# Optimization experiments

Measured on AMD Instinct MI355X. Metric: run time of the kernel, lower is better.

The kernel has to match this reference:

```python
import jax, jax.numpy as jnp
import numpy as np

DIM_V = 512
NUM_HEADS = 8
LN_EPS = 1e-5


def _layernorm(x):
    # LayerNorm over last dim, no affine (simplified_layer_norm=True)
    mu = jnp.mean(x, axis=-1, keepdims=True)
    var = jnp.mean(jnp.square(x - mu), axis=-1, keepdims=True)
    return (x - mu) * jax.lax.rsqrt(var + LN_EPS)


def setup_inputs() -> dict:
    key = jax.random.key(0)
    ks = jax.random.split(key, 12)
    B, Nq, Nk, dQ, dK, dV = 16, 1024, 1024, 512, 512, DIM_V
    s = 0.02
    return {
        "Q": jax.random.normal(ks[0], (B, Nq, dQ), jnp.float32),
        "K": jax.random.normal(ks[1], (B, Nk, dK), jnp.float32),
        "Wq": jax.random.normal(ks[2], (dQ, dV), jnp.float32) * s,
        "bq": jnp.zeros((dV,), jnp.float32),
        "Wk": jax.random.normal(ks[3], (dK, dV), jnp.float32) * s,
        "bk": jnp.zeros((dV,), jnp.float32),
        "Wv": jax.random.normal(ks[4], (dK, dV), jnp.float32) * s,
        "bv": jnp.zeros((dV,), jnp.float32),
        "Wo": jax.random.normal(ks[5], (dV, dV), jnp.float32) * s,
        "bo": jnp.zeros((dV,), jnp.float32),
    }


def reference(Q, K, Wq, bq, Wk, bk, Wv, bv, Wo, bo):
    H = NUM_HEADS
    dh = DIM_V // H
    q = Q @ Wq + bq            # [B, Nq, dV]
    k = K @ Wk + bk            # [B, Nk, dV]
    v = K @ Wv + bv            # [B, Nk, dV]
    B, Nq, _ = q.shape
    Nk = k.shape[1]
    qh = q.reshape(B, Nq, H, dh)
    kh = k.reshape(B, Nk, H, dh)
    vh = v.reshape(B, Nk, H, dh)
    # NOTE: faithful to source — scale by sqrt(dim_V), not sqrt(head_dim)
    scores = jnp.einsum('bqhd,bkhd->bhqk', qh, kh) / jnp.sqrt(jnp.asarray(DIM_V, q.dtype))
    A = jax.nn.softmax(scores, axis=-1)                    # [B, H, Nq, Nk]
    attn = jnp.einsum('bhqk,bkhd->bqhd', A, vh).reshape(B, Nq, DIM_V)
    O = q + attn               # residual with projected Q
    O = _layernorm(O)          # ln0 (no affine)
    O = O + jax.nn.gelu(O @ Wo + bo, approximate=False)
    O = _layernorm(O)          # ln1 (no affine)
    return O
```

## Files before the change

kernel.cpp:

```cpp
#include <hip/hip_runtime.h>
#include <hip/hip_bf16.h>
#include <math.h>

typedef __bf16 bf16;
typedef __bf16 bf16x8 __attribute__((ext_vector_type(8)));
typedef float  f32x4  __attribute__((ext_vector_type(4)));
typedef float  f32x16 __attribute__((ext_vector_type(16)));
typedef unsigned u32x4 __attribute__((ext_vector_type(4)));

#define MFMA16(a,b,c) __builtin_amdgcn_mfma_f32_16x16x32_bf16((a),(b),(c),0,0,0)
#define MFMA32(a,b,c) __builtin_amdgcn_mfma_f32_32x32x16_bf16((a),(b),(c),0,0,0)
#define KSCALE 0.0637587159f

__device__ __forceinline__ void async16p(const void* g, void* l) {
    __builtin_amdgcn_global_load_lds((const __attribute__((address_space(1))) void*)g,
                                     (__attribute__((address_space(3))) void*)l,
                                     16, 0, 0);
}

__device__ __forceinline__ float fexp2(float x) {
#if __has_builtin(__builtin_amdgcn_exp2f)
    return __builtin_amdgcn_exp2f(x);
#else
    return exp2f(x);
#endif
}

__device__ __forceinline__ unsigned pkbf(float a, float b) {
    union { bf16 h[2]; unsigned u; } x;
    x.h[0] = (bf16)a; x.h[1] = (bf16)b; return x.u;
}

__device__ __forceinline__ void plswap(unsigned &a, unsigned &b) {
#if __has_builtin(__builtin_amdgcn_permlane32_swap)
    auto r = __builtin_amdgcn_permlane32_swap((int)a, (int)b, false, false);
    a = (unsigned)r[0]; b = (unsigned)r[1];
#else
    unsigned sa = (unsigned)__shfl_xor((int)a, 32);
    unsigned sb = (unsigned)__shfl_xor((int)b, 32);
    bool hi = (threadIdx.x & 32) != 0;
    unsigned na = hi ? sb : a;
    unsigned nb = hi ? b  : sa;
    a = na; b = nb;
#endif
}

__global__ __launch_bounds__(256) void prep_w_kernel(
    const float* __restrict__ Wq, const float* __restrict__ Wk,
    const float* __restrict__ Wv, const float* __restrict__ Wo,
    bf16* __restrict__ WqT, bf16* __restrict__ WkT,
    bf16* __restrict__ WvT, bf16* __restrict__ WoT,
    float* __restrict__ csum)
{
    __shared__ float tile[32][33];
    const int bx = blockIdx.x;
    const float* W; bf16* T;
    switch (bx >> 8) {
      case 0: W=Wq; T=WqT; break;
      case 1: W=Wk; T=WkT; break;
      case 2: W=Wv; T=WvT; break;
      default: W=Wo; T=WoT; break;
    }
    const int rest = bx & 255;
    const int k0 = (rest & 15) * 32, n0 = (rest >> 4) * 32;
    const int tx = threadIdx.x & 31, ty = threadIdx.x >> 5;
    float sacc = 0.f;
    #pragma unroll
    for (int i=0;i<32;i+=8) {
        float v = W[(size_t)(k0+ty+i)*512 + n0+tx];
        tile[ty+i][tx] = v;
        sacc += v;
    }
    __syncthreads();
    #pragma unroll
    for (int i=0;i<32;i+=8)
        T[(size_t)(n0+ty+i)*512 + k0+tx] = (bf16)tile[tx][ty+i];
    if ((bx >> 8) == 3) {
        __syncthreads();
        tile[ty][tx] = sacc;
        __syncthreads();
        if (ty == 0) {
            float s = 0.f;
            #pragma unroll
            for (int j=0;j<8;j++) s += tile[j][tx];
            atomicAdd(&csum[n0+tx], s);
        }
    }
}

__global__ __launch_bounds__(256, 2) void gemm_proj_kernel(
    const float* __restrict__ Qf, const float* __restrict__ Kf,
    const bf16* __restrict__ WqT, const bf16* __restrict__ WkT,
    const bf16* __restrict__ WvT,
    const float* __restrict__ bq, const float* __restrict__ bk,
    const float* __restrict__ bv,
    bf16* __restrict__ qbb, bf16* __restrict__ kbb, bf16* __restrict__ vT)
{
    __shared__ __align__(16) char smem[65536];
    float* As32 = (float*)smem;
    bf16*  Bs   = (bf16*)(smem + 32768);
    bf16*  Lt   = (bf16*)smem;

    const int x = blockIdx.x;
    const bool isQ = (x < 256);
    int m0, n0;
    const float* A; const bf16 *BT0, *BT1; const float *bb0, *bb1;
    if (isQ) {
        m0 = (x >> 1) * 128; n0 = (x & 1) * 128;
        A = Qf; BT0 = WqT + (size_t)n0*512; BT1 = WqT + (size_t)(n0+256)*512;
        bb0 = bq + n0; bb1 = bq + n0 + 256;
    } else {
        int r = x - 256;
        m0 = (r >> 2) * 128; n0 = (r & 3) * 128;
        A = Kf; BT0 = WkT + (size_t)n0*512; BT1 = WvT + (size_t)n0*512;
        bb0 = bk + n0; bb1 = bv + n0;
    }

    const int tid = threadIdx.x;
    const int lane = tid & 63, wave = tid >> 6;
    const int qd = lane >> 4, lr = lane & 15;
    const int wm = (wave & 1) * 64, wn = (wave >> 1) * 64;

    const float* gA = A + (size_t)(m0 + (tid>>3))*512 + (((tid&7)^((tid>>3)&7))*4);
    const int bgr = ((tid & 3) ^ ((tid >> 3) & 3)) * 8;
    const bf16* gB0 = BT0 + (size_t)(tid>>2)*512 + bgr;
    const bf16* gB1 = BT1 + (size_t)(tid>>2)*512 + bgr;

    f32x4 acc[2][4][4];
    #pragma unroll
    for (int p=0;p<2;p++)
      #pragma unroll
      for (int i=0;i<4;i++)
        #pragma unroll
        for (int j=0;j<4;j++) acc[p][i][j] = (f32x4){0,0,0,0};

    auto stage = [&](int buf, int k0) {
        float* lA = As32 + buf*4096 + wave*256;
        #pragma unroll
        for (int i=0;i<4;i++)
            async16p(gA + k0 + (size_t)i*32*512, lA + i*1024);
        bf16* lB0 = Bs + buf*8192 + wave*512;
        async16p(gB0 + k0,                  lB0);
        async16p(gB0 + k0 + (size_t)64*512, lB0 + 2048);
        bf16* lB1 = Bs + buf*8192 + 4096 + wave*512;
        async16p(gB1 + k0,                  lB1);
        async16p(gB1 + k0 + (size_t)64*512, lB1 + 2048);
    };

    stage(0, 0);
    for (int t = 0; t < 16; ++t) {
        const int cur = t & 1;
        __builtin_amdgcn_sched_barrier(0);
        __builtin_amdgcn_s_barrier();
        if (t < 15) {
            stage(cur ^ 1, (t+1)*32);
            asm volatile("s_waitcnt vmcnt(8)" ::: "memory");
        } else {
            asm volatile("s_waitcnt vmcnt(0)" ::: "memory");
        }
        __builtin_amdgcn_s_barrier();

        const float* Ab = As32 + cur*4096;
        const bf16*  Bb = Bs   + cur*8192;
        bf16x8 af[4], bfr[2][4];
        #pragma unroll
        for (int mi=0;mi<4;mi++) {
            int row = wm + mi*16 + lr;
            f32x4 f0 = *(f32x4*)(Ab + row*32 + (((qd*2  )^(lr&7))*4));
            f32x4 f1 = *(f32x4*)(Ab + row*32 + (((qd*2+1)^(lr&7))*4));
            bf16x8 a;
            a[0]=(bf16)f0[0]; a[1]=(bf16)f0[1]; a[2]=(bf16)f0[2]; a[3]=(bf16)f0[3];
            a[4]=(bf16)f1[0]; a[5]=(bf16)f1[1]; a[6]=(bf16)f1[2]; a[7]=(bf16)f1[3];
            af[mi] = a;
        }
        #pragma unroll
        for (int p=0;p<2;p++)
          #pragma unroll
          for (int ni=0;ni<4;ni++)
            bfr[p][ni] = *(bf16x8*)(Bb + p*4096 + (wn+ni*16+lr)*32
                                       + ((qd^((lr>>1)&3))*8));
        #pragma unroll
        for (int p=0;p<2;p++)
          #pragma unroll
          for (int mi=0;mi<4;mi++)
            #pragma unroll
            for (int ni=0;ni<4;ni++)
              acc[p][mi][ni] = MFMA16(af[mi], bfr[p][ni], acc[p][mi][ni]);
    }

    if (isQ) {
        #pragma unroll
        for (int p=0;p<2;p++) {
            const float* bb = p ? bb1 : bb0;
            #pragma unroll
            for (int ni=0;ni<4;ni++) {
                int nl = wn + ni*16 + lr;
                int n = n0 + p*256 + nl;
                float bv0 = bb[nl];
                #pragma unroll
                for (int mi=0;mi<4;mi++) {
                    int mb = m0 + wm + mi*16 + qd*4;
                    #pragma unroll
                    for (int r=0;r<4;r++)
                        qbb[(size_t)(mb+r)*512 + n] = (bf16)(acc[p][mi][ni][r] + bv0);
                }
            }
        }
    } else {
        #pragma unroll
        for (int ni=0;ni<4;ni++) {
            int nl = wn + ni*16 + lr;
            int n = n0 + nl;
            float bv0 = bb0[nl];
            #pragma unroll
            for (int mi=0;mi<4;mi++) {
                int mb = m0 + wm + mi*16 + qd*4;
                #pragma unroll
                for (int r=0;r<4;r++)
                    kbb[(size_t)(mb+r)*512 + n] = (bf16)((acc[0][mi][ni][r] + bv0)*KSCALE);
            }
        }
        const int b = m0 >> 10, tok0 = m0 & 1023;
        const int row = tid >> 2, ch = tid & 3;
        #pragma unroll
        for (int half = 0; half < 2; ++half) {
            __syncthreads();
            if ((wn >> 6) == half) {
                #pragma unroll
                for (int ni=0;ni<4;ni++) {
                    int nl = ni*16 + lr;
                    float bvv = bb1[half*64 + nl];
                    #pragma unroll
                    for (int mi=0;mi<4;mi++)
                      #pragma unroll
                      for (int r=0;r<4;r++) {
                        int col = wm + mi*16 + qd*4 + r;
                        Lt[nl*128 + ((((col>>3)^(nl&7))<<3) | (col&7))]
                            = (bf16)(acc[1][mi][ni][r] + bvv);
                      }
                }
            }
            __syncthreads();
            const int h = (n0 >> 6) + half;
            bf16* dst = vT + ((size_t)((b*8 + h)*64 + row))*1024 + tok0 + ch*32;
            #pragma unroll
            for (int s=0;s<4;s++) {
                int g = (ch*4 + s) ^ (row & 7);
                *(uint4*)(dst + s*8) = *(uint4*)(Lt + row*128 + g*8);
            }
        }
    }
}

__global__ __launch_bounds__(256, 4) void attn_kernel(
    const bf16* __restrict__ qb, const bf16* __restrict__ kb,
    const bf16* __restrict__ vT, bf16* __restrict__ attnb)
{
    const int x = blockIdx.x;
    const int qt = x >> 7, h = x & 7, b = (x & 127) >> 3;
    const int tid = threadIdx.x, lane = tid & 63, wave = tid >> 6;
    const int l = lane & 31, hi = lane >> 5;
    const int q0w = qt*128 + wave*32;

    __shared__ __align__(16) bf16 kv[2][2][4096];
    __shared__ float ls[4][32];

    bf16x8 aq[4];
    {
        const bf16* qrow = qb + ((size_t)(b*1024 + q0w + l))*512 + h*64 + hi*8;
        #pragma unroll
        for (int st=0; st<4; ++st) aq[st] = *(const bf16x8*)(qrow + st*16);
    }

    const int srow = lane >> 3;
    const int sgA  = (lane & 7) ^ srow ^ wave;
    const int sgB  = sgA ^ 4;
    const bf16* kg0 = kb + ((size_t)(b*1024 + wave*8 + srow))*512      + h*64 + sgA*8;
    const bf16* kg1 = kb + ((size_t)(b*1024 + wave*8 + srow + 32))*512 + h*64 + sgB*8;
    const bf16* vg0 = vT + ((size_t)((b*8 + h)*64 + wave*8 + srow))*1024      + sgA*8;
    const bf16* vg1 = vT + ((size_t)((b*8 + h)*64 + wave*8 + srow + 32))*1024 + sgB*8;

    auto stage = [&](int buf, int t) {
        const size_t ko = (size_t)t*64*512;
        async16p(kg0 + ko,     &kv[buf][0][wave*512]);
        async16p(kg1 + ko,     &kv[buf][0][2048 + wave*512]);
        async16p(vg0 + t*64,   &kv[buf][1][wave*512]);
        async16p(vg1 + t*64,   &kv[buf][1][2048 + wave*512]);
    };

    f32x16 accO[2];
    accO[0] = (f32x16)0.f; accO[1] = (f32x16)0.f;
    float lsum = 0.f;
    const int kx = (l & 7) ^ (l >> 3);

    stage(0, 0);
    for (int t=0; t<16; ++t) {
        const int cur = t & 1;
        __builtin_amdgcn_sched_barrier(0);
        __builtin_amdgcn_s_barrier();
        if (t < 15) {
            stage(cur ^ 1, t + 1);
            asm volatile("s_waitcnt vmcnt(4)" ::: "memory");
        } else {
            asm volatile("s_waitcnt vmcnt(0)" ::: "memory");
        }
        __builtin_amdgcn_s_barrier();

        const bf16* Ks = kv[cur][0];
        const bf16* Vs = kv[cur][1];

        u32x4 paf[4];
        #pragma unroll
        for (int kb2=0; kb2<2; ++kb2) {
            f32x16 sT = (f32x16)0.f;
            __builtin_amdgcn_s_setprio(1);
            #pragma unroll
            for (int st=0; st<4; ++st) {
                bf16x8 kf = *(const bf16x8*)(Ks + (kb2*32 + l)*64
                               + (((st*2 + hi) ^ kx ^ (kb2<<2))*8));
                sT = MFMA32(kf, aq[st], sT);
            }
            __builtin_amdgcn_s_setprio(0);
            unsigned u[8];
            #pragma unroll
            for (int m=0; m<8; ++m) {
                float e0 = fexp2(sT[2*m]);
                float e1 = fexp2(sT[2*m+1]);
                lsum += e0 + e1;
                u[m] = pkbf(e0, e1);
            }
            #pragma unroll
            for (int sb=0; sb<2; ++sb) {
                unsigned a0=u[4*sb], a1=u[4*sb+1], a2=u[4*sb+2], a3=u[4*sb+3];
                plswap(a0, a2);
                plswap(a1, a3);
                paf[kb2*2 + sb] = (u32x4){a0, a1, a2, a3};
            }
        }
        __builtin_amdgcn_s_setprio(1);
        #pragma unroll
        for (int db=0; db<2; ++db) {
            f32x16 a = accO[db];
            #pragma unroll
            for (int st=0; st<4; ++st) {
                bf16x8 vf = *(const bf16x8*)(Vs + (db*32 + l)*64
                               + (((st*2 + hi) ^ kx ^ (db<<2))*8));
                u32x4 pp = paf[st];
                bf16x8 pf = *(bf16x8*)&pp;
                a = MFMA32(pf, vf, a);
            }
            accO[db] = a;
        }
        __builtin_amdgcn_s_setprio(0);
    }

    lsum += __shfl_xor(lsum, 32);
    ls[wave][l] = lsum;
    __syncthreads();

    #pragma unroll
    for (int g=0; g<4; ++g) {
        f32x4 lv = *(const f32x4*)(&ls[wave][g*8 + hi*4]);
        f32x4 inv;
        #pragma unroll
        for (int i=0;i<4;i++) inv[i] = 1.f / lv[i];
        #pragma unroll
        for (int db=0; db<2; ++db) {
            #pragma unroll
            for (int i=0;i<4;i++) {
                int r = g*4 + i;
                int qrow = q0w + g*8 + hi*4 + i;
                size_t idx = ((size_t)(b*1024 + qrow))*512 + h*64 + db*32 + l;
                float o = accO[db][r] * inv[i] + (float)qb[idx];
                attnb[idx] = (bf16)o;
            }
        }
    }
}

__global__ __launch_bounds__(256, 4) void gemm_o_kernel(
    const bf16* __restrict__ attnb, const bf16* __restrict__ WoT,
    const float* __restrict__ bo, const float* __restrict__ csum,
    bf16* __restrict__ xb)
{
    __shared__ __align__(16) char smem[24576];
    __shared__ float2 rs[64];
    bf16* As = (bf16*)smem;
    bf16* Bs = (bf16*)(smem + 8192);
    const int m0 = blockIdx.x * 64, n0 = blockIdx.y * 128;
    const int tid = threadIdx.x;
    const int lane = tid & 63, wave = tid >> 6;
    const int qd = lane >> 4, lr = lane & 15;
    const int wm = (wave & 1) * 32, wn = (wave >> 1) * 64;

    const int bgr = ((tid & 3) ^ ((tid >> 3) & 3)) * 8;
    const bf16* gA = attnb + (size_t)(m0 + (tid>>2))*512 + bgr;
    const bf16* gB = WoT   + (size_t)(n0 + (tid>>2))*512 + bgr;

    f32x4 acc[2][4];
    #pragma unroll
    for (int i=0;i<2;i++)
      #pragma unroll
      for (int j=0;j<4;j++) acc[i][j] = (f32x4){0,0,0,0};
    float s1[2] = {0.f, 0.f}, s2[2] = {0.f, 0.f};

    auto stage = [&](int buf, int k0) {
        async16p(gA + k0,                  As + buf*2048 + wave*512);
        bf16* lB = Bs + buf*4096 + wave*512;
        async16p(gB + k0,                  lB);
        async16p(gB + k0 + (size_t)64*512, lB + 2048);
    };

    stage(0, 0);
    for (int t = 0; t < 16; ++t) {
        const int cur = t & 1;
        __builtin_amdgcn_sched_barrier(0);
        __builtin_amdgcn_s_barrier();
        if (t < 15) {
            stage(cur ^ 1, (t+1)*32);
            asm volatile("s_waitcnt vmcnt(3)" ::: "memory");
        } else {
            asm volatile("s_waitcnt vmcnt(0)" ::: "memory");
        }
        __builtin_amdgcn_s_barrier();

        const bf16* Ab = As + cur*2048;
        const bf16* Bb = Bs + cur*4096;
        bf16x8 af[2], bfr[4];
        #pragma unroll
        for (int mi=0;mi<2;mi++) {
            af[mi] = *(bf16x8*)(Ab + (wm+mi*16+lr)*32 + ((qd^((lr>>1)&3))*8));
            #pragma unroll
            for (int j=0;j<8;j++) {
                float v = (float)af[mi][j];
                s1[mi] += v;
                s2[mi] += v*v;
            }
        }
        #pragma unroll
        for (int ni=0;ni<4;ni++)
            bfr[ni] = *(bf16x8*)(Bb + (wn+ni*16+lr)*32 + ((qd^((lr>>1)&3))*8));
        #pragma unroll
        for (int mi=0;mi<2;mi++)
          #pragma unroll
          for (int ni=0;ni<4;ni++)
            acc[mi][ni] = MFMA16(af[mi], bfr[ni], acc[mi][ni]);
    }

    #pragma unroll
    for (int mi=0;mi<2;mi++) {
        s1[mi] += __shfl_xor(s1[mi], 16); s2[mi] += __shfl_xor(s2[mi], 16);
        s1[mi] += __shfl_xor(s1[mi], 32); s2[mi] += __shfl_xor(s2[mi], 32);
    }
    if (wave < 2 && qd == 0) {
        #pragma unroll
        for (int mi=0;mi<2;mi++) {
            float mu  = s1[mi] * (1.f/512.f);
            float var = s2[mi] * (1.f/512.f) - mu*mu;
            rs[wm + mi*16 + lr] = make_float2(mu, rsqrtf(var + 1e-5f));
        }
    }
    __syncthreads();

    float csn[4], bon[4];
    #pragma unroll
    for (int ni=0;ni<4;ni++) {
        int n = n0 + wn + ni*16 + lr;
        csn[ni] = csum[n];
        bon[ni] = bo[n];
    }
    #pragma unroll
    for (int mi=0;mi<2;mi++) {
        #pragma unroll
        for (int r=0;r<4;r++) {
            int rl = wm + mi*16 + qd*4 + r;
            int row = m0 + rl;
            float2 st = rs[rl];
            float mu = st.x, rstd = st.y;
            #pragma unroll
            for (int ni=0;ni<4;ni++) {
                int n = n0 + wn + ni*16 + lr;
                float g = rstd*acc[mi][ni][r] - rstd*mu*csn[ni] + bon[ni];
                float gelu = 0.5f * g * (1.f + erff(g * 0.70710678118654752f));
                size_t idx = (size_t)row*512 + n;
                float lnx = ((float)attnb[idx] - mu) * rstd;
                xb[idx] = (bf16)(lnx + gelu);
            }
        }
    }
}

__global__ __launch_bounds__(256) void ln1_kernel(
    const bf16* __restrict__ xb, float* __restrict__ out)
{
    const int wave = threadIdx.x >> 6, lane = threadIdx.x & 63;
    const int row = blockIdx.x*4 + wave;
    const size_t base = (size_t)row*512 + lane*8;
    bf16x8 xv = *(const bf16x8*)(xb + base);
    float x[8];
    #pragma unroll
    for (int i=0;i<8;i++) x[i] = (float)xv[i];
    float s1 = 0.f, s2 = 0.f;
    #pragma unroll
    for (int i=0;i<8;i++){ s1 += x[i]; s2 += x[i]*x[i]; }
    #pragma unroll
    for (int off=1; off<64; off<<=1) { s1 += __shfl_xor(s1, off); s2 += __shfl_xor(s2, off); }
    float mu  = s1 * (1.f/512.f);
    float var = s2 * (1.f/512.f) - mu*mu;
    float rstd = rsqrtf(var + 1e-5f);
    float4 o0 = {(x[0]-mu)*rstd,(x[1]-mu)*rstd,(x[2]-mu)*rstd,(x[3]-mu)*rstd};
    float4 o1 = {(x[4]-mu)*rstd,(x[5]-mu)*rstd,(x[6]-mu)*rstd,(x[7]-mu)*rstd};
    *(float4*)(out + base)     = o0;
    *(float4*)(out + base + 4) = o1;
}

extern "C" void kernel_launch(void* const* d_in, const int* in_sizes, int n_in,
                              void* d_out, int out_size, void* d_ws, size_t ws_size,
                              hipStream_t stream)
{
    (void)in_sizes; (void)n_in; (void)out_size; (void)ws_size;
    const float* Q  = (const float*)d_in[0];
    const float* K  = (const float*)d_in[1];
    const float* Wq = (const float*)d_in[2];
    const float* bq = (const float*)d_in[3];
    const float* Wk = (const float*)d_in[4];
    const float* bk = (const float*)d_in[5];
    const float* Wv = (const float*)d_in[6];
    const float* bv = (const float*)d_in[7];
    const float* Wo = (const float*)d_in[8];
    const float* bo = (const float*)d_in[9];
    float* out = (float*)d_out;

    const size_t nTok = (size_t)16*1024*512;
    char* p = (char*)d_ws;
    auto alloc = [&](size_t bytes)->char* {
        char* r = p; p += (bytes + 255) & ~(size_t)255; return r;
    };
    bf16*   WqT   = (bf16*)alloc(512*512*2);
    bf16*   WkT   = (bf16*)alloc(512*512*2);
    bf16*   WvT   = (bf16*)alloc(512*512*2);
    bf16*   WoT   = (bf16*)alloc(512*512*2);
    bf16*   qbb   = (bf16*)alloc(nTok*2);
    bf16*   kbb   = (bf16*)alloc(nTok*2);
    bf16*   vT    = (bf16*)alloc(nTok*2);
    bf16*   attnb = (bf16*)alloc(nTok*2);
    bf16*   xb    = (bf16*)alloc(nTok*2);
    float*  csum  = (float*)alloc(512*4);

    hipMemsetAsync(csum, 0, 512*sizeof(float), stream);
    prep_w_kernel<<<1024, 256, 0, stream>>>(Wq, Wk, Wv, Wo, WqT, WkT, WvT, WoT, csum);
    gemm_proj_kernel<<<768, 256, 0, stream>>>(Q, K, WqT, WkT, WvT,
                                              bq, bk, bv, qbb, kbb, vT);
    attn_kernel<<<dim3(1024), 256, 0, stream>>>(qbb, kbb, vT, attnb);
    gemm_o_kernel<<<dim3(256,4), 256, 0, stream>>>(attnb, WoT, bo, csum, xb);
    ln1_kernel<<<4096, 256, 0, stream>>>(xb, out);
}
```

Baseline: 244.0 us.

## Fuse final LayerNorm into output GEMM with full-row tiles

The output-projection GEMM now computes all 512 columns per 64-row tile with 512 threads and 144KB of dynamic LDS, so each block holds complete rows. That allows the second LayerNorm to be computed in the epilogue through a cross-wave reduction in shared memory, which removes the separate ln1 kernel and the bf16 intermediate round trip through global memory. The cost is lower occupancy and only 256 blocks, which may underfill the GPU, plus much larger per-block LDS use.

New measurement: 252.4 us. +3.4%, slower.

```diff
diff --git a/kernel.cpp b/kernel.cpp
--- a/kernel.cpp
+++ b/kernel.cpp
@@ -378,73 +378,80 @@
     }
 }
 
-__global__ __launch_bounds__(256, 4) void gemm_o_kernel(
+__global__ __launch_bounds__(512, 2) void gemm_o_kernel(
     const bf16* __restrict__ attnb, const bf16* __restrict__ WoT,
     const float* __restrict__ bo, const float* __restrict__ csum,
-    bf16* __restrict__ xb)
+    float* __restrict__ out)
 {
-    __shared__ __align__(16) char smem[24576];
+    extern __shared__ char smem[];
+    bf16* As = (bf16*)smem;
+    bf16* Bs = (bf16*)(smem + 16384);
     __shared__ float2 rs[64];
-    bf16* As = (bf16*)smem;
-    bf16* Bs = (bf16*)(smem + 8192);
-    const int m0 = blockIdx.x * 64, n0 = blockIdx.y * 128;
+    __shared__ float  ws1[4][64], ws2[4][64];
+
+    const int m0 = blockIdx.x * 64;
     const int tid = threadIdx.x;
     const int lane = tid & 63, wave = tid >> 6;
     const int qd = lane >> 4, lr = lane & 15;
-    const int wm = (wave & 1) * 32, wn = (wave >> 1) * 64;
-
-    const int bgr = ((tid & 3) ^ ((tid >> 3) & 3)) * 8;
-    const bf16* gA = attnb + (size_t)(m0 + (tid>>2))*512 + bgr;
-    const bf16* gB = WoT   + (size_t)(n0 + (tid>>2))*512 + bgr;
-
-    f32x4 acc[2][4];
+    const int wm = (wave & 1) * 32, wn = (wave >> 1) * 128;
+
+    const int srow8 = lane >> 3;
+    const int sg    = (lane & 7) ^ srow8;
+    const bf16* gA = attnb + (size_t)(m0 + wave*8 + srow8)*512 + sg*8;
+    const bf16* gB = WoT   + (size_t)(wave*64 + srow8)*512 + sg*8;
+
+    f32x4 acc[2][8];
     #pragma unroll
     for (int i=0;i<2;i++)
       #pragma unroll
-      for (int j=0;j<4;j++) acc[i][j] = (f32x4){0,0,0,0};
-    float s1[2] = {0.f, 0.f}, s2[2] = {0.f, 0.f};
+      for (int j=0;j<8;j++) acc[i][j] = (f32x4){0,0,0,0};
+    float s1[2] = {0.f,0.f}, s2[2] = {0.f,0.f};
 
     auto stage = [&](int buf, int k0) {
-        async16p(gA + k0,                  As + buf*2048 + wave*512);
-        bf16* lB = Bs + buf*4096 + wave*512;
-        async16p(gB + k0,                  lB);
-        async16p(gB + k0 + (size_t)64*512, lB + 2048);
+        async16p(gA + k0, As + buf*4096 + wave*512);
+        bf16* lB = Bs + buf*32768 + wave*4096;
+        #pragma unroll
+        for (int j=0;j<8;j++)
+            async16p(gB + k0 + (size_t)j*8*512, lB + j*512);
     };
 
     stage(0, 0);
-    for (int t = 0; t < 16; ++t) {
+    for (int t = 0; t < 8; ++t) {
         const int cur = t & 1;
         __builtin_amdgcn_sched_barrier(0);
         __builtin_amdgcn_s_barrier();
-        if (t < 15) {
-            stage(cur ^ 1, (t+1)*32);
-            asm volatile("s_waitcnt vmcnt(3)" ::: "memory");
+        if (t < 7) {
+            stage(cur ^ 1, (t+1)*64);
+            asm volatile("s_waitcnt vmcnt(9)" ::: "memory");
         } else {
             asm volatile("s_waitcnt vmcnt(0)" ::: "memory");
         }
         __builtin_amdgcn_s_barrier();
 
-        const bf16* Ab = As + cur*2048;
-        const bf16* Bb = Bs + cur*4096;
-        bf16x8 af[2], bfr[4];
-        #pragma unroll
-        for (int mi=0;mi<2;mi++) {
-            af[mi] = *(bf16x8*)(Ab + (wm+mi*16+lr)*32 + ((qd^((lr>>1)&3))*8));
-            #pragma unroll
-            for (int j=0;j<8;j++) {
-                float v = (float)af[mi][j];
-                s1[mi] += v;
-                s2[mi] += v*v;
-            }
-        }
-        #pragma unroll
-        for (int ni=0;ni<4;ni++)
-            bfr[ni] = *(bf16x8*)(Bb + (wn+ni*16+lr)*32 + ((qd^((lr>>1)&3))*8));
-        #pragma unroll
-        for (int mi=0;mi<2;mi++)
-          #pragma unroll
-          for (int ni=0;ni<4;ni++)
-            acc[mi][ni] = MFMA16(af[mi], bfr[ni], acc[mi][ni]);
+        const bf16* Ab = As + cur*4096;
+        const bf16* Bb = Bs + cur*32768;
+        #pragma unroll
+        for (int kk=0; kk<2; ++kk) {
+            bf16x8 af[2];
+            #pragma unroll
+            for (int mi=0;mi<2;mi++) {
+                int row = wm + mi*16 + lr;
+                af[mi] = *(bf16x8*)(Ab + row*64 + (((kk*4+qd)^(lr&7))*8));
+                #pragma unroll
+                for (int j=0;j<8;j++) {
+                    float v = (float)af[mi][j];
+                    s1[mi] += v; s2[mi] += v*v;
+                }
+            }
+            #pragma unroll
+            for (int ni=0;ni<8;ni++) {
+                int brow = wn + ni*16 + lr;
+                bf16x8 bfr = *(bf16x8*)(Bb + brow*64 + (((kk*4+qd)^(lr&7))*8));
+                #pragma unroll
+                for (int mi=0;mi<2;mi++)
+                    acc[mi][ni] = MFMA16(af[mi], bfr, acc[mi][ni]);
+            }
+        }
     }
 
     #pragma unroll
@@ -452,6 +459,7 @@
         s1[mi] += __shfl_xor(s1[mi], 16); s2[mi] += __shfl_xor(s2[mi], 16);
         s1[mi] += __shfl_xor(s1[mi], 32); s2[mi] += __shfl_xor(s2[mi], 32);
     }
+    __syncthreads();
     if (wave < 2 && qd == 0) {
         #pragma unroll
         for (int mi=0;mi<2;mi++) {
@@ -462,56 +470,80 @@
     }
     __syncthreads();
 
-    float csn[4], bon[4];
-    #pragma unroll
-    for (int ni=0;ni<4;ni++) {
-        int n = n0 + wn + ni*16 + lr;
+    float csn[8], bon[8];
+    #pragma unroll
+    for (int ni=0;ni<8;ni++) {
+        int n = wn + ni*16 + lr;
         csn[ni] = csum[n];
         bon[ni] = bo[n];
     }
+
+    unsigned xvp[2][8][2];
+    float t1[2][4] = {{0,0,0,0},{0,0,0,0}}, t2[2][4] = {{0,0,0,0},{0,0,0,0}};
+    #pragma unroll
+    for (int mi=0;mi<2;mi++) {
+        #pragma unroll
+        for (int ni=0;ni<8;ni++) {
+            float xq[4];
+            #pragma unroll
+            for (int r=0;r<4;r++) {
+                int rl = wm + mi*16 + qd*4 + r;
+                float2 st = rs[rl];
+                float mu0 = st.x, rstd0 = st.y;
+                int n = wn + ni*16 + lr;
+                float g = rstd0*acc[mi][ni][r] - rstd0*mu0*csn[ni] + bon[ni];
+                float gelu = 0.5f * g * (1.f + erff(g * 0.70710678118654752f));
+                float lnx = ((float)attnb[(size_t)(m0+rl)*512 + n] - mu0) * rstd0;
+                float xv = lnx + gelu;
+                t1[mi][r] += xv; t2[mi][r] += xv*xv;
+                xq[r] = xv;
+            }
+            xvp[mi][ni][0] = pkbf(xq[0], xq[1]);
+            xvp[mi][ni][1] = pkbf(xq[2], xq[3]);
+        }
+    }
+
+    #pragma unroll
+    for (int mi=0;mi<2;mi++)
+      #pragma unroll
+      for (int r=0;r<4;r++)
+        #pragma unroll
+        for (int off=1; off<16; off<<=1) {
+            t1[mi][r] += __shfl_xor(t1[mi][r], off);
+            t2[mi][r] += __shfl_xor(t2[mi][r], off);
+        }
+    if (lr == 0) {
+        #pragma unroll
+        for (int mi=0;mi<2;mi++)
+          #pragma unroll
+          for (int r=0;r<4;r++) {
+            int rl = wm + mi*16 + qd*4 + r;
+            ws1[wave>>1][rl] = t1[mi][r];
+            ws2[wave>>1][rl] = t2[mi][r];
+          }
+    }
+    __syncthreads();
+
     #pragma unroll
     for (int mi=0;mi<2;mi++) {
         #pragma unroll
         for (int r=0;r<4;r++) {
             int rl = wm + mi*16 + qd*4 + r;
-            int row = m0 + rl;
-            float2 st = rs[rl];
-            float mu = st.x, rstd = st.y;
-            #pragma unroll
-            for (int ni=0;ni<4;ni++) {
-                int n = n0 + wn + ni*16 + lr;
-                float g = rstd*acc[mi][ni][r] - rstd*mu*csn[ni] + bon[ni];
-                float gelu = 0.5f * g * (1.f + erff(g * 0.70710678118654752f));
-                size_t idx = (size_t)row*512 + n;
-                float lnx = ((float)attnb[idx] - mu) * rstd;
-                xb[idx] = (bf16)(lnx + gelu);
-            }
-        }
-    }
-}
-
-__global__ __launch_bounds__(256) void ln1_kernel(
-    const bf16* __restrict__ xb, float* __restrict__ out)
-{
-    const int wave = threadIdx.x >> 6, lane = threadIdx.x & 63;
-    const int row = blockIdx.x*4 + wave;
-    const size_t base = (size_t)row*512 + lane*8;
-    bf16x8 xv = *(const bf16x8*)(xb + base);
-    float x[8];
-    #pragma unroll
-    for (int i=0;i<8;i++) x[i] = (float)xv[i];
-    float s1 = 0.f, s2 = 0.f;
-    #pragma unroll
-    for (int i=0;i<8;i++){ s1 += x[i]; s2 += x[i]*x[i]; }
-    #pragma unroll
-    for (int off=1; off<64; off<<=1) { s1 += __shfl_xor(s1, off); s2 += __shfl_xor(s2, off); }
-    float mu  = s1 * (1.f/512.f);
-    float var = s2 * (1.f/512.f) - mu*mu;
-    float rstd = rsqrtf(var + 1e-5f);
-    float4 o0 = {(x[0]-mu)*rstd,(x[1]-mu)*rstd,(x[2]-mu)*rstd,(x[3]-mu)*rstd};
-    float4 o1 = {(x[4]-mu)*rstd,(x[5]-mu)*rstd,(x[6]-mu)*rstd,(x[7]-mu)*rstd};
-    *(float4*)(out + base)     = o0;
-    *(float4*)(out + base + 4) = o1;
+            float S1 = ws1[0][rl] + ws1[1][rl] + ws1[2][rl] + ws1[3][rl];
+            float S2 = ws2[0][rl] + ws2[1][rl] + ws2[2][rl] + ws2[3][rl];
+            float mu1  = S1 * (1.f/512.f);
+            float var1 = S2 * (1.f/512.f) - mu1*mu1;
+            float rstd1 = rsqrtf(var1 + 1e-5f);
+            float* orow = out + (size_t)(m0+rl)*512;
+            #pragma unroll
+            for (int ni=0;ni<8;ni++) {
+                union { unsigned u; bf16 h[2]; } w;
+                w.u = xvp[mi][ni][r>>1];
+                float xv = (float)w.h[r&1];
+                orow[wn + ni*16 + lr] = (xv - mu1) * rstd1;
+            }
+        }
+    }
 }
 
 extern "C" void kernel_launch(void* const* d_in, const int* in_sizes, int n_in,
@@ -544,14 +576,19 @@
     bf16*   kbb   = (bf16*)alloc(nTok*2);
     bf16*   vT    = (bf16*)alloc(nTok*2);
     bf16*   attnb = (bf16*)alloc(nTok*2);
-    bf16*   xb    = (bf16*)alloc(nTok*2);
     float*  csum  = (float*)alloc(512*4);
+
+    static bool attrSet = false;
+    if (!attrSet) {
+        hipFuncSetAttribute((const void*)gemm_o_kernel,
+                            hipFuncAttributeMaxDynamicSharedMemorySize, 147456);
+        attrSet = true;
+    }
 
     hipMemsetAsync(csum, 0, 512*sizeof(float), stream);
     prep_w_kernel<<<1024, 256, 0, stream>>>(Wq, Wk, Wv, Wo, WqT, WkT, WvT, WoT, csum);
     gemm_proj_kernel<<<768, 256, 0, stream>>>(Q, K, WqT, WkT, WvT,
                                               bq, bk, bv, qbb, kbb, vT);
     attn_kernel<<<dim3(1024), 256, 0, stream>>>(qbb, kbb, vT, attnb);
-    gemm_o_kernel<<<dim3(256,4), 256, 0, stream>>>(attnb, WoT, bo, csum, xb);
-    ln1_kernel<<<4096, 256, 0, stream>>>(xb, out);
-}
+    gemm_o_kernel<<<256, 512, 147456, stream>>>(attnb, WoT, bo, csum, out);
+}
```
